# Kernel optimization log

Hardware: AMD Instinct MI355X
Metric: run time of the kernel (lower is better)

The kernel has to match this reference:

```python
import jax, jax.numpy as jnp
import numpy as np

N_Q_HEADS = 16
N_KV_HEADS = 4
HEAD_DIM = 128
SLIDING_WINDOW = 1024
ROPE_BASE = 1024


def _rope_tables(L, dim):
    # half-truncate RoPE: first dim//4 freqs geometric, next dim//4 zero
    freqs = (1.0 / ROPE_BASE) ** jnp.linspace(0.0, 1.0, num=dim // 4)
    freqs = jnp.concatenate([freqs, jnp.zeros(dim // 4, dtype=freqs.dtype)])
    theta = jnp.arange(L, dtype=jnp.float32)[:, None] * freqs[None, :]  # (L, dim/2)
    cos = jnp.cos(theta)[None, :, None, :]  # (1, L, 1, dim/2)
    sin = jnp.sin(theta)[None, :, None, :]
    return cos, sin


def _rotate(x, cos, sin):
    # x: (B, L, H, D)
    x1, x2 = jnp.split(x, 2, axis=-1)
    return jnp.concatenate([x1 * cos + x2 * sin, -x1 * sin + x2 * cos], axis=-1)


def setup_inputs() -> dict:
    key = jax.random.key(0)
    k1, k2, k3, k4 = jax.random.split(key, 4)
    B, L, D = 1, 2048, 2048
    qkv_dim = (N_Q_HEADS + 2 * N_KV_HEADS) * HEAD_DIM  # 3072
    return {
        "x": jax.random.normal(k1, (B, L, D), dtype=jnp.float32),
        "Wqkv": jax.random.normal(k2, (D, qkv_dim), dtype=jnp.float32) * (D ** -0.5),
        "Wo": jax.random.normal(k3, (N_Q_HEADS * HEAD_DIM, D), dtype=jnp.float32) * ((N_Q_HEADS * HEAD_DIM) ** -0.5),
        "s": jax.random.normal(k4, (1, N_Q_HEADS), dtype=jnp.float32) * 0.1,
    }


def reference(x, Wqkv, Wo, s):
    B, L, D = x.shape
    H, QM, hd = N_KV_HEADS, N_Q_HEADS // N_KV_HEADS, HEAD_DIM

    proj = x @ Wqkv  # (B, L, (Hq + 2*Hkv) * hd)
    q, k, v = jnp.split(proj, (N_Q_HEADS * hd, (N_Q_HEADS + N_KV_HEADS) * hd), axis=-1)

    cos, sin = _rope_tables(L, hd)
    q = _rotate(q.reshape(B, L, -1, hd), cos, sin).reshape(B, L, H, QM, hd)
    k = _rotate(k.reshape(B, L, H, hd), cos, sin)
    v = v.reshape(B, L, H, hd)

    sm_scale = 1.0 / jnp.sqrt(jnp.float32(hd))
    q_pos = jnp.arange(L)[None, :, None]
    k_pos = jnp.arange(L)[None, None, :]
    causal = q_pos >= k_pos                       # (1, L, L)
    window = q_pos < k_pos + SLIDING_WINDOW       # index % 2 == 0 -> window active
    mask = causal & window

    # (B, H, M, Lq, Lk) attention logits
    attn = jnp.einsum("bqhmd,bkhd->bhmqk", q, k) * sm_scale
    # NOTE: faithful to source: -inf placed WHERE mask is True
    attn = jnp.where(mask, -jnp.inf, attn)

    sink = jnp.broadcast_to(s.reshape(B, H, QM, 1, 1), (B, H, QM, L, 1))
    w = jax.nn.softmax(jnp.concatenate([attn, sink], axis=-1), axis=-1)[..., :-1]

    out = jnp.einsum("bhmqk,bkhd->bqhmd", w, v).reshape(B, L, -1)
    return out @ Wo
```

## Files before the change

### kernel.cpp

```cpp
#include <hip/hip_runtime.h>
#include <hip/hip_bf16.h>
#include <math.h>

typedef __bf16 bf16;
typedef __bf16 bf16x8 __attribute__((ext_vector_type(8)));
typedef __bf16 bf16x4v __attribute__((ext_vector_type(4)));
typedef short s16x4 __attribute__((ext_vector_type(4)));
typedef float f32x4 __attribute__((ext_vector_type(4)));

#define GLD16(gp, lp) __builtin_amdgcn_global_load_lds( \
    (__attribute__((address_space(1))) void*)(void*)(gp), \
    (__attribute__((address_space(3))) void*)(lp), 16, 0, 0)

#define L_SEQ 2048
#define D_MODEL 2048
#define QKV_N 3072
#define HD 128
#define QSCALE 0.1275310242959836f
#define LOG2E 1.4426950408889634f

__global__ __launch_bounds__(256) void prep(const float* __restrict__ x,
                                            const float* __restrict__ Wqkv,
                                            const float* __restrict__ Wo,
                                            bf16* __restrict__ xb,
                                            bf16* __restrict__ wqkvT,
                                            bf16* __restrict__ woT) {
    __shared__ float tile[32][33];
    int bid = blockIdx.x;
    if (bid < 4096) {
        int idx = (bid * 256 + threadIdx.x) * 4;
        float4 f = *(const float4*)(x + idx);
        bf16x4v o;
        o.x = (bf16)f.x; o.y = (bf16)f.y; o.z = (bf16)f.z; o.w = (bf16)f.w;
        *(bf16x4v*)(xb + idx) = o;
        return;
    }
    bid -= 4096;
    const float* src; bf16* dst; long ld_s, ld_d; int bx, by;
    if (bid < 6144) { bx = bid % 96; by = bid / 96; src = Wqkv; dst = wqkvT; ld_s = QKV_N; ld_d = D_MODEL; }
    else { bid -= 6144; bx = bid & 63; by = bid >> 6; src = Wo; dst = woT; ld_s = D_MODEL; ld_d = D_MODEL; }
    const int tx = threadIdx.x & 31, ty = threadIdx.x >> 5;
    const long c = bx * 32 + tx, r0 = by * 32;
#pragma unroll
    for (int i = 0; i < 4; ++i)
        tile[ty + i * 8][tx] = src[(r0 + ty + i * 8) * ld_s + c];
    __syncthreads();
    const long c0 = bx * 32;
#pragma unroll
    for (int i = 0; i < 4; ++i)
        dst[(c0 + ty + i * 8) * ld_d + r0 + tx] = (bf16)tile[tx][ty + i * 8];
}

__global__ __launch_bounds__(256, 3) void gemm_qkv(const bf16* __restrict__ A,
                                                   const bf16* __restrict__ Bt,
                                                   bf16* __restrict__ Qb,
                                                   bf16* __restrict__ Kb,
                                                   bf16* __restrict__ Vtb) {
    constexpr int KDIM = D_MODEL;
    __shared__ __align__(16) bf16 As[2][64 * 64];
    __shared__ __align__(16) bf16 Bs[2][128 * 64];
    const int tid = threadIdx.x;
    const int wid = tid >> 6, lane = tid & 63;
    const int quad = lane >> 4, l15 = lane & 15;
    const int wm = wid & 1, wn = wid >> 1;
    const int head = blockIdx.x;
    const long m0 = (long)blockIdx.y * 64, n0 = (long)head * 128;

    f32x4 acc[2][4];
#pragma unroll
    for (int i = 0; i < 2; ++i)
#pragma unroll
        for (int j = 0; j < 4; ++j) acc[i][j] = (f32x4){0.f, 0.f, 0.f, 0.f};

    const int srow8 = lane >> 3;
    const int schunk = lane & 7;

    auto stage = [&](int k0, int buf) {
#pragma unroll
        for (int ii = 0; ii < 2; ++ii) {
            const int rowb = wid * 16 + ii * 8;
            const int row = rowb + srow8;
            const int gcol = (schunk ^ (row & 7)) * 8;
            GLD16(A + (m0 + row) * KDIM + k0 + gcol, &As[buf][rowb * 64]);
        }
#pragma unroll
        for (int ii = 0; ii < 4; ++ii) {
            const int rowb = wid * 32 + ii * 8;
            const int row = rowb + srow8;
            const int gcol = (schunk ^ (row & 7)) * 8;
            GLD16(Bt + (n0 + row) * KDIM + k0 + gcol, &Bs[buf][rowb * 64]);
        }
    };
    stage(0, 0);

    for (int k0 = 0; k0 < KDIM; k0 += 64) {
        __syncthreads();
        if (k0 + 64 < KDIM) stage(k0 + 64, ((k0 >> 6) + 1) & 1);
        const int buf = (k0 >> 6) & 1;
#pragma unroll
        for (int ks = 0; ks < 2; ++ks) {
            const int pos = ((ks * 4 + quad) ^ (l15 & 7)) * 8;
            bf16x8 af[2], bfr[4];
#pragma unroll
            for (int i = 0; i < 2; ++i)
                af[i] = *(const bf16x8*)&As[buf][(wm * 32 + i * 16 + l15) * 64 + pos];
#pragma unroll
            for (int j = 0; j < 4; ++j)
                bfr[j] = *(const bf16x8*)&Bs[buf][(j * 32 + wn * 16 + l15) * 64 + pos];
#pragma unroll
            for (int i = 0; i < 2; ++i)
#pragma unroll
                for (int j = 0; j < 4; ++j)
                    acc[i][j] = __builtin_amdgcn_mfma_f32_16x16x32_bf16(af[i], bfr[j], acc[i][j], 0, 0, 0);
        }
    }

    if (head < 20) {
        const float sc = head < 16 ? QSCALE : 1.0f;
        bf16* dst = head < 16 ? Qb + (long)head * L_SEQ * HD
                              : Kb + (long)(head - 16) * L_SEQ * HD;
        const int d0 = wn * 16 + l15;
        const float freq = exp2f((float)d0 * (-10.0f / 31.0f));
        const int d1 = 32 + wn * 16 + l15;
#pragma unroll
        for (int i = 0; i < 2; ++i)
#pragma unroll
            for (int r = 0; r < 4; ++r) {
                const long row = m0 + wm * 32 + i * 16 + quad * 4 + r;
                float sn, cs;
                sincosf((float)row * freq, &sn, &cs);
                const float x1 = acc[i][0][r], x2 = acc[i][2][r];
                bf16* p = dst + row * HD;
                p[d0]      = (bf16)((x1 * cs + x2 * sn) * sc);
                p[d0 + 64] = (bf16)((x2 * cs - x1 * sn) * sc);
                p[d1]      = (bf16)(acc[i][1][r] * sc);
                p[d1 + 64] = (bf16)(acc[i][3][r] * sc);
            }
    } else {
        bf16* dst = Vtb + (long)(head - 20) * HD * L_SEQ;
#pragma unroll
        for (int i = 0; i < 2; ++i) {
            const long m = m0 + wm * 32 + i * 16 + quad * 4;
#pragma unroll
            for (int j = 0; j < 4; ++j) {
                const int d = j * 32 + wn * 16 + l15;
                bf16x4v vv;
#pragma unroll
                for (int r = 0; r < 4; ++r) vv[r] = (bf16)acc[i][j][r];
                *(bf16x4v*)(dst + (long)d * L_SEQ + m) = vv;
            }
        }
    }
}

__global__ __launch_bounds__(256, 3) void gemm_out(const bf16* __restrict__ A,
                                                   const bf16* __restrict__ Bt,
                                                   float* __restrict__ C) {
    constexpr int KDIM = D_MODEL;
    __shared__ __align__(16) bf16 As[2][64 * 64];
    __shared__ __align__(16) bf16 Bs[2][128 * 64];
    const int tid = threadIdx.x;
    const int wid = tid >> 6, lane = tid & 63;
    const int quad = lane >> 4, l15 = lane & 15;
    const int wm = wid & 1, wn = wid >> 1;
    const long m0 = (long)blockIdx.y * 64, n0 = (long)blockIdx.x * 128;

    f32x4 acc[2][4];
#pragma unroll
    for (int i = 0; i < 2; ++i)
#pragma unroll
        for (int j = 0; j < 4; ++j) acc[i][j] = (f32x4){0.f, 0.f, 0.f, 0.f};

    const int srow8 = lane >> 3;
    const int schunk = lane & 7;

    auto stage = [&](int k0, int buf) {
#pragma unroll
        for (int ii = 0; ii < 2; ++ii) {
            const int rowb = wid * 16 + ii * 8;
            const int row = rowb + srow8;
            const int gcol = (schunk ^ (row & 7)) * 8;
            GLD16(A + (m0 + row) * KDIM + k0 + gcol, &As[buf][rowb * 64]);
        }
#pragma unroll
        for (int ii = 0; ii < 4; ++ii) {
            const int rowb = wid * 32 + ii * 8;
            const int row = rowb + srow8;
            const int gcol = (schunk ^ (row & 7)) * 8;
            GLD16(Bt + (n0 + row) * KDIM + k0 + gcol, &Bs[buf][rowb * 64]);
        }
    };
    stage(0, 0);

    for (int k0 = 0; k0 < KDIM; k0 += 64) {
        __syncthreads();
        if (k0 + 64 < KDIM) stage(k0 + 64, ((k0 >> 6) + 1) & 1);
        const int buf = (k0 >> 6) & 1;
#pragma unroll
        for (int ks = 0; ks < 2; ++ks) {
            const int pos = ((ks * 4 + quad) ^ (l15 & 7)) * 8;
            bf16x8 af[2], bfr[4];
#pragma unroll
            for (int i = 0; i < 2; ++i)
                af[i] = *(const bf16x8*)&As[buf][(wm * 32 + i * 16 + l15) * 64 + pos];
#pragma unroll
            for (int j = 0; j < 4; ++j)
                bfr[j] = *(const bf16x8*)&Bs[buf][(j * 32 + wn * 16 + l15) * 64 + pos];
#pragma unroll
            for (int i = 0; i < 2; ++i)
#pragma unroll
                for (int j = 0; j < 4; ++j)
                    acc[i][j] = __builtin_amdgcn_mfma_f32_16x16x32_bf16(af[i], bfr[j], acc[i][j], 0, 0, 0);
        }
    }

#pragma unroll
    for (int i = 0; i < 2; ++i)
#pragma unroll
        for (int j = 0; j < 4; ++j) {
            const long row = m0 + wm * 32 + i * 16 + quad * 4;
            const long col = n0 + j * 32 + wn * 16 + l15;
#pragma unroll
            for (int r = 0; r < 4; ++r)
                C[(row + r) * (long)D_MODEL + col] = acc[i][j][r];
        }
}

__global__ __launch_bounds__(256, 2) void attn_p(const bf16* __restrict__ Qb,
                                                 const bf16* __restrict__ Kb,
                                                 const bf16* __restrict__ Vtb,
                                                 bf16* __restrict__ Opart,
                                                 float* __restrict__ lpart) {
    __shared__ __align__(1024) char smem[65536];

    const int bid = blockIdx.x;
    int t, hq, half;
    if (bid < 256) { t = bid >> 5; hq = (bid & 31) >> 1; half = bid & 1; }
    else { int b2 = bid - 256; t = 8 + (b2 >> 5); hq = (b2 & 31) >> 1; half = b2 & 1; }
    const int h = hq >> 2;
    const int q0 = t * 128;
    const int tid = threadIdx.x;
    const int w = tid >> 6;
    const int lane = tid & 63;
    const int quad = lane >> 4, l15 = lane & 15;

    const bf16* Qg = Qb + (long)hq * L_SEQ * HD;
    const bf16* Kg = Kb + (long)h * L_SEQ * HD;
    const bf16* Vg = Vtb + (long)h * HD * L_SEQ;

    bf16x8 qb[2][4];
#pragma unroll
    for (int rf = 0; rf < 2; ++rf)
#pragma unroll
        for (int kkd = 0; kkd < 4; ++kkd)
            qb[rf][kkd] = *(const bf16x8*)(Qg + (long)(q0 + w * 32 + rf * 16 + l15) * HD
                                              + kkd * 32 + quad * 8);

    f32x4 oaccT[2][8];
#pragma unroll
    for (int rf = 0; rf < 2; ++rf)
#pragma unroll
        for (int j = 0; j < 8; ++j) oaccT[rf][j] = (f32x4){0.f, 0.f, 0.f, 0.f};
    float lacc[2] = {0.f, 0.f};

    const int locnt = (2 * t - 14 > 0) ? (2 * t - 14) : 0;
    const int n = locnt + 32 - 2 * t;
    const int cnt = n >> 1;

    auto ktile = [&](int idx) {
        const int i = 2 * idx + half;
        return (i < locnt) ? i : (2 * t + (i - locnt));
    };

    auto stage = [&](int idx, int buf) {
        const int k0 = ktile(idx) * 64;
        bf16* Ksb  = (bf16*)(smem + buf * 32768);
        bf16* Vtsb = (bf16*)(smem + buf * 32768 + 16384);
#pragma unroll
        for (int ii = 0; ii < 4; ++ii) {
            int rowb = w * 16 + ii * 4;
            int row = rowb + quad;
            GLD16(Kg + (long)(k0 + row) * HD + ((l15 ^ (row & 7)) * 8), &Ksb[rowb * 128]);
        }
#pragma unroll
        for (int ii = 0; ii < 4; ++ii) {
            int rowb = w * 32 + ii * 8;
            int row = rowb + (lane >> 3);
            GLD16(Vg + (long)row * L_SEQ + k0 + (((lane & 7) ^ (row & 7)) * 8), &Vtsb[rowb * 64]);
        }
    };

    stage(0, 0);

    for (int it = 0; it < cnt; ++it) {
        __syncthreads();
        if (it + 1 < cnt) stage(it + 1, (it + 1) & 1);

        const int kt = ktile(it);
        const int k0 = kt * 64;
        const bf16* Ks  = (const bf16*)(smem + (it & 1) * 32768);
        const bf16* Vts = (const bf16*)(smem + (it & 1) * 32768 + 16384);

        f32x4 sacc[2][4];
#pragma unroll
        for (int kb = 0; kb < 4; ++kb) {
            bf16x8 ka[4];
#pragma unroll
            for (int kkd = 0; kkd < 4; ++kkd)
                ka[kkd] = *(const bf16x8*)&Ks[(kb * 16 + l15) * 128 +
                                              (((kkd * 4 + quad) ^ (l15 & 7)) * 8)];
#pragma unroll
            for (int rf = 0; rf < 2; ++rf) {
                f32x4 acc = (f32x4){0.f, 0.f, 0.f, 0.f};
#pragma unroll
                for (int kkd = 0; kkd < 4; ++kkd)
                    acc = __builtin_amdgcn_mfma_f32_16x16x32_bf16(ka[kkd], qb[rf][kkd], acc, 0, 0, 0);
                sacc[rf][kb] = acc;
            }
        }

        const bool bnd = (kt == 2 * t) || (kt == 2 * t + 1) ||
                         (kt == 2 * t - 15) || (kt == 2 * t - 16);
        s16x4 pb[2][4];
#pragma unroll
        for (int rf = 0; rf < 2; ++rf) {
            const int qq = q0 + w * 32 + rf * 16 + l15;
#pragma unroll
            for (int kb = 0; kb < 4; ++kb) {
#pragma unroll
                for (int r = 0; r < 4; ++r) {
                    float v = sacc[rf][kb][r];
                    if (bnd) {
                        const int kk = k0 + kb * 16 + quad * 4 + r;
                        if (!((kk > qq) || (kk <= qq - 1024))) v = -1e30f;
                    }
                    const float p = exp2f(v);
                    lacc[rf] += p;
                    bf16 hp = (bf16)p;
                    pb[rf][kb][r] = __builtin_bit_cast(short, hp);
                }
            }
        }

#pragma unroll
        for (int j = 0; j < 8; ++j) {
            const int drow = j * 16 + l15;
#pragma unroll
            for (int kq = 0; kq < 4; ++kq) {
                const int pc = ((kq * 2 + (quad >> 1)) ^ (l15 & 7));
                s16x4 va = *(const s16x4*)((const char*)&Vts[drow * 64] + pc * 16 + (quad & 1) * 8);
#pragma unroll
                for (int rf = 0; rf < 2; ++rf)
                    oaccT[rf][j] = __builtin_amdgcn_mfma_f32_16x16x16bf16_1k(
                        va, pb[rf][kq], oaccT[rf][j], 0, 0, 0);
            }
        }
    }

#pragma unroll
    for (int rf = 0; rf < 2; ++rf) {
        lacc[rf] += __shfl_xor(lacc[rf], 16, 64);
        lacc[rf] += __shfl_xor(lacc[rf], 32, 64);
    }

    bf16* Od = Opart + (long)bid * 16384;
#pragma unroll
    for (int rf = 0; rf < 2; ++rf) {
        const int ql = w * 32 + rf * 16 + l15;
#pragma unroll
        for (int j = 0; j < 8; ++j) {
            bf16x4v ov;
#pragma unroll
            for (int r = 0; r < 4; ++r) ov[r] = (bf16)oaccT[rf][j][r];
            *(bf16x4v*)(Od + ql * 128 + j * 16 + quad * 4) = ov;
        }
        if (quad == 0) lpart[bid * 128 + ql] = lacc[rf];
    }
}

__global__ __launch_bounds__(256) void attn_combine(const bf16* __restrict__ Opart,
                                                    const float* __restrict__ lpart,
                                                    const float* __restrict__ sink,
                                                    bf16* __restrict__ attnb) {
    const int job = blockIdx.x >> 3, sub = blockIdx.x & 7;
    const int t = job >> 4, hq = job & 15;
    const int bid0 = (t < 8) ? (t * 32 + hq * 2) : (256 + (t - 8) * 32 + hq * 2);
    const int bid1 = bid0 + 1;
    const int e = sub * 2048 + threadIdx.x * 8;
    const int q = e >> 7, d0 = e & 127;
    bf16x8 o0 = *(const bf16x8*)(Opart + (long)bid0 * 16384 + q * 128 + d0);
    bf16x8 o1 = *(const bf16x8*)(Opart + (long)bid1 * 16384 + q * 128 + d0);
    const float l = lpart[bid0 * 128 + q] + lpart[bid1 * 128 + q] +
                    exp2f(sink[hq] * LOG2E);
    const float inv = 1.0f / l;
    bf16x8 ov;
#pragma unroll
    for (int r = 0; r < 8; ++r)
        ov[r] = (bf16)(((float)o0[r] + (float)o1[r]) * inv);
    *(bf16x8*)(attnb + (long)(t * 128 + q) * D_MODEL + hq * 128 + d0) = ov;
}

extern "C" void kernel_launch(void* const* d_in, const int* in_sizes, int n_in,
                              void* d_out, int out_size, void* d_ws, size_t ws_size,
                              hipStream_t stream) {
    (void)in_sizes; (void)n_in; (void)out_size; (void)ws_size;
    const float* x    = (const float*)d_in[0];
    const float* Wqkv = (const float*)d_in[1];
    const float* Wo   = (const float*)d_in[2];
    const float* s    = (const float*)d_in[3];
    float* out = (float*)d_out;

    char* ws = (char*)d_ws;
    bf16* xb    = (bf16*)ws;
    bf16* wqkvT = (bf16*)(ws + 8388608);
    bf16* Qb    = (bf16*)(ws + 20971520);
    bf16* Kb    = (bf16*)(ws + 29360128);
    bf16* Vtb   = (bf16*)(ws + 31457280);
    bf16* woT   = (bf16*)(ws + 33554432);
    bf16* attnb = (bf16*)(ws + 41943040);
    bf16* Opart = (bf16*)ws;
    float* lpart = (float*)(ws + 16777216);

    prep<<<14336, 256, 0, stream>>>(x, Wqkv, Wo, xb, wqkvT, woT);

    gemm_qkv<<<dim3(QKV_N / 128, L_SEQ / 64), 256, 0, stream>>>(
        xb, wqkvT, Qb, Kb, Vtb);

    attn_p<<<512, 256, 0, stream>>>(Qb, Kb, Vtb, Opart, lpart);

    attn_combine<<<2048, 256, 0, stream>>>(Opart, lpart, s, attnb);

    gemm_out<<<dim3(D_MODEL / 128, L_SEQ / 64), 256, 0, stream>>>(
        attnb, woT, out);
}
```

Before: 218.4 us.

## Split attention KV range four ways with 32-key tiles and higher occupancy

Each attention job is now split across four blocks instead of two, using 32-key tiles and half the shared memory so that four blocks can be resident per CU. The partial outputs are spread over the output buffer and the workspace, and the combine kernel sums four partials. s_setprio is raised around the MFMA sections so waves in the matrix phase get issue priority. The aim is more parallelism and better latency hiding, paid for with more partial-output traffic and a larger per-tile overhead share.

```diff
diff --git a/kernel.cpp b/kernel.cpp
--- a/kernel.cpp
+++ b/kernel.cpp
@@ -226,17 +226,17 @@
         }
 }
 
-__global__ __launch_bounds__(256, 2) void attn_p(const bf16* __restrict__ Qb,
+__global__ __launch_bounds__(256, 4) void attn_p(const bf16* __restrict__ Qb,
                                                  const bf16* __restrict__ Kb,
                                                  const bf16* __restrict__ Vtb,
-                                                 bf16* __restrict__ Opart,
+                                                 bf16* __restrict__ O0,
+                                                 bf16* __restrict__ O1,
                                                  float* __restrict__ lpart) {
-    __shared__ __align__(1024) char smem[65536];
-
-    const int bid = blockIdx.x;
-    int t, hq, half;
-    if (bid < 256) { t = bid >> 5; hq = (bid & 31) >> 1; half = bid & 1; }
-    else { int b2 = bid - 256; t = 8 + (b2 >> 5); hq = (b2 & 31) >> 1; half = b2 & 1; }
+    __shared__ __align__(1024) char smem[32768];
+
+    const int pbid = blockIdx.x;
+    const int job = pbid >> 2, qtr = pbid & 3;
+    const int t = job >> 4, hq = job & 15;
     const int h = hq >> 2;
     const int q0 = t * 128;
     const int tid = threadIdx.x;
@@ -263,30 +263,31 @@
         for (int j = 0; j < 8; ++j) oaccT[rf][j] = (f32x4){0.f, 0.f, 0.f, 0.f};
     float lacc[2] = {0.f, 0.f};
 
-    const int locnt = (2 * t - 14 > 0) ? (2 * t - 14) : 0;
-    const int n = locnt + 32 - 2 * t;
-    const int cnt = n >> 1;
+    const int locnt = (4 * t - 28 > 0) ? (4 * t - 28) : 0;
+    const int n32 = locnt + 64 - 4 * t;
+    const int cnt = (n32 - qtr + 3) >> 2;
 
     auto ktile = [&](int idx) {
-        const int i = 2 * idx + half;
-        return (i < locnt) ? i : (2 * t + (i - locnt));
+        const int i = 4 * idx + qtr;
+        return (i < locnt) ? i : (4 * t + (i - locnt));
     };
 
     auto stage = [&](int idx, int buf) {
-        const int k0 = ktile(idx) * 64;
-        bf16* Ksb  = (bf16*)(smem + buf * 32768);
-        bf16* Vtsb = (bf16*)(smem + buf * 32768 + 16384);
-#pragma unroll
-        for (int ii = 0; ii < 4; ++ii) {
-            int rowb = w * 16 + ii * 4;
-            int row = rowb + quad;
+        const int k0 = ktile(idx) * 32;
+        bf16* Ksb  = (bf16*)(smem + buf * 16384);
+        bf16* Vtsb = (bf16*)(smem + buf * 16384 + 8192);
+#pragma unroll
+        for (int ii = 0; ii < 2; ++ii) {
+            const int rowb = w * 8 + ii * 4;
+            const int row = rowb + quad;
             GLD16(Kg + (long)(k0 + row) * HD + ((l15 ^ (row & 7)) * 8), &Ksb[rowb * 128]);
         }
 #pragma unroll
-        for (int ii = 0; ii < 4; ++ii) {
-            int rowb = w * 32 + ii * 8;
-            int row = rowb + (lane >> 3);
-            GLD16(Vg + (long)row * L_SEQ + k0 + (((lane & 7) ^ (row & 7)) * 8), &Vtsb[rowb * 64]);
+        for (int ii = 0; ii < 2; ++ii) {
+            const int rowb = w * 32 + ii * 16;
+            const int row = rowb + (lane >> 2);
+            GLD16(Vg + (long)row * L_SEQ + k0 + (((lane & 3) ^ ((row >> 1) & 3)) * 8),
+                  &Vtsb[rowb * 32]);
         }
     };
 
@@ -297,13 +298,14 @@
         if (it + 1 < cnt) stage(it + 1, (it + 1) & 1);
 
         const int kt = ktile(it);
-        const int k0 = kt * 64;
-        const bf16* Ks  = (const bf16*)(smem + (it & 1) * 32768);
-        const bf16* Vts = (const bf16*)(smem + (it & 1) * 32768 + 16384);
-
-        f32x4 sacc[2][4];
-#pragma unroll
-        for (int kb = 0; kb < 4; ++kb) {
+        const int k0 = kt * 32;
+        const bf16* Ks  = (const bf16*)(smem + (it & 1) * 16384);
+        const bf16* Vts = (const bf16*)(smem + (it & 1) * 16384 + 8192);
+
+        f32x4 sacc[2][2];
+        __builtin_amdgcn_s_setprio(1);
+#pragma unroll
+        for (int kb = 0; kb < 2; ++kb) {
             bf16x8 ka[4];
 #pragma unroll
             for (int kkd = 0; kkd < 4; ++kkd)
@@ -318,15 +320,16 @@
                 sacc[rf][kb] = acc;
             }
         }
-
-        const bool bnd = (kt == 2 * t) || (kt == 2 * t + 1) ||
-                         (kt == 2 * t - 15) || (kt == 2 * t - 16);
-        s16x4 pb[2][4];
+        __builtin_amdgcn_s_setprio(0);
+
+        const bool bnd = (kt >= 4 * t && kt < 4 * t + 4) ||
+                         (kt >= 4 * t - 32 && kt <= 4 * t - 29);
+        s16x4 pb[2][2];
 #pragma unroll
         for (int rf = 0; rf < 2; ++rf) {
             const int qq = q0 + w * 32 + rf * 16 + l15;
 #pragma unroll
-            for (int kb = 0; kb < 4; ++kb) {
+            for (int kb = 0; kb < 2; ++kb) {
 #pragma unroll
                 for (int r = 0; r < 4; ++r) {
                     float v = sacc[rf][kb][r];
@@ -342,19 +345,21 @@
             }
         }
 
+        __builtin_amdgcn_s_setprio(1);
 #pragma unroll
         for (int j = 0; j < 8; ++j) {
             const int drow = j * 16 + l15;
 #pragma unroll
-            for (int kq = 0; kq < 4; ++kq) {
-                const int pc = ((kq * 2 + (quad >> 1)) ^ (l15 & 7));
-                s16x4 va = *(const s16x4*)((const char*)&Vts[drow * 64] + pc * 16 + (quad & 1) * 8);
+            for (int kq = 0; kq < 2; ++kq) {
+                const int pc = (kq * 2 + (quad >> 1)) ^ ((drow >> 1) & 3);
+                s16x4 va = *(const s16x4*)((const char*)&Vts[drow * 32] + pc * 16 + (quad & 1) * 8);
 #pragma unroll
                 for (int rf = 0; rf < 2; ++rf)
                     oaccT[rf][j] = __builtin_amdgcn_mfma_f32_16x16x16bf16_1k(
                         va, pb[rf][kq], oaccT[rf][j], 0, 0, 0);
             }
         }
+        __builtin_amdgcn_s_setprio(0);
     }
 
 #pragma unroll
@@ -363,7 +368,8 @@
         lacc[rf] += __shfl_xor(lacc[rf], 32, 64);
     }
 
-    bf16* Od = Opart + (long)bid * 16384;
+    bf16* Od = (pbid < 512) ? O0 + (long)pbid * 16384
+                            : O1 + (long)(pbid - 512) * 16384;
 #pragma unroll
     for (int rf = 0; rf < 2; ++rf) {
         const int ql = w * 32 + rf * 16 + l15;
@@ -374,29 +380,37 @@
             for (int r = 0; r < 4; ++r) ov[r] = (bf16)oaccT[rf][j][r];
             *(bf16x4v*)(Od + ql * 128 + j * 16 + quad * 4) = ov;
         }
-        if (quad == 0) lpart[bid * 128 + ql] = lacc[rf];
-    }
-}
-
-__global__ __launch_bounds__(256) void attn_combine(const bf16* __restrict__ Opart,
+        if (quad == 0) lpart[pbid * 128 + ql] = lacc[rf];
+    }
+}
+
+__global__ __launch_bounds__(256) void attn_combine(const bf16* __restrict__ O0,
+                                                    const bf16* __restrict__ O1,
                                                     const float* __restrict__ lpart,
                                                     const float* __restrict__ sink,
                                                     bf16* __restrict__ attnb) {
     const int job = blockIdx.x >> 3, sub = blockIdx.x & 7;
     const int t = job >> 4, hq = job & 15;
-    const int bid0 = (t < 8) ? (t * 32 + hq * 2) : (256 + (t - 8) * 32 + hq * 2);
-    const int bid1 = bid0 + 1;
+    const bf16* Ob = (job < 128) ? O0 + (long)job * 65536
+                                 : O1 + (long)(job - 128) * 65536;
     const int e = sub * 2048 + threadIdx.x * 8;
     const int q = e >> 7, d0 = e & 127;
-    bf16x8 o0 = *(const bf16x8*)(Opart + (long)bid0 * 16384 + q * 128 + d0);
-    bf16x8 o1 = *(const bf16x8*)(Opart + (long)bid1 * 16384 + q * 128 + d0);
-    const float l = lpart[bid0 * 128 + q] + lpart[bid1 * 128 + q] +
-                    exp2f(sink[hq] * LOG2E);
+    float acc[8];
+#pragma unroll
+    for (int r = 0; r < 8; ++r) acc[r] = 0.f;
+    float l = exp2f(sink[hq] * LOG2E);
+#pragma unroll
+    for (int s = 0; s < 4; ++s) {
+        bf16x8 o = *(const bf16x8*)(Ob + (long)s * 16384 + q * 128 + d0);
+#pragma unroll
+        for (int r = 0; r < 8; ++r) acc[r] += (float)o[r];
+        l += lpart[(job * 4 + s) * 128 + q];
+    }
     const float inv = 1.0f / l;
     bf16x8 ov;
 #pragma unroll
     for (int r = 0; r < 8; ++r)
-        ov[r] = (bf16)(((float)o0[r] + (float)o1[r]) * inv);
+        ov[r] = (bf16)(acc[r] * inv);
     *(bf16x8*)(attnb + (long)(t * 128 + q) * D_MODEL + hq * 128 + d0) = ov;
 }
 
@@ -418,7 +432,8 @@
     bf16* Vtb   = (bf16*)(ws + 31457280);
     bf16* woT   = (bf16*)(ws + 33554432);
     bf16* attnb = (bf16*)(ws + 41943040);
-    bf16* Opart = (bf16*)ws;
+    bf16* Opart0 = (bf16*)out;
+    bf16* Opart1 = (bf16*)ws;
     float* lpart = (float*)(ws + 16777216);
 
     prep<<<14336, 256, 0, stream>>>(x, Wqkv, Wo, xb, wqkvT, woT);
@@ -426,9 +441,9 @@
     gemm_qkv<<<dim3(QKV_N / 128, L_SEQ / 64), 256, 0, stream>>>(
         xb, wqkvT, Qb, Kb, Vtb);
 
-    attn_p<<<512, 256, 0, stream>>>(Qb, Kb, Vtb, Opart, lpart);
-
-    attn_combine<<<2048, 256, 0, stream>>>(Opart, lpart, s, attnb);
+    attn_p<<<1024, 256, 0, stream>>>(Qb, Kb, Vtb, Opart0, Opart1, lpart);
+
+    attn_combine<<<2048, 256, 0, stream>>>(Opart0, Opart1, lpart, s, attnb);
 
     gemm_out<<<dim3(D_MODEL / 128, L_SEQ / 64), 256, 0, stream>>>(
         attnb, woT, out);
```

Result: slower. 309.2 us (+41.6%).

## Use 8 waves per attention block with 16 query rows each and MFMA priority

Applied to the files above, without the earlier changes.

The attention kernel now runs 512 threads per block. Each of its 8 waves handles 16 query rows instead of 32, which halves the per-thread register arrays for Q fragments, accumulators and probabilities and lets more waves be resident. K/V staging is split across the larger thread count. s_setprio is raised around the MFMA phases so waves doing matrix work get scheduler priority over the softmax phase. The trade-off is that each K fragment read from LDS is now reused for one query fragment instead of two, so LDS traffic per FLOP doubles.

```diff
diff --git a/kernel.cpp b/kernel.cpp
--- a/kernel.cpp
+++ b/kernel.cpp
@@ -226,7 +226,7 @@
         }
 }
 
-__global__ __launch_bounds__(256, 2) void attn_p(const bf16* __restrict__ Qb,
+__global__ __launch_bounds__(512, 4) void attn_p(const bf16* __restrict__ Qb,
                                                  const bf16* __restrict__ Kb,
                                                  const bf16* __restrict__ Vtb,
                                                  bf16* __restrict__ Opart,
@@ -248,20 +248,16 @@
     const bf16* Kg = Kb + (long)h * L_SEQ * HD;
     const bf16* Vg = Vtb + (long)h * HD * L_SEQ;
 
-    bf16x8 qb[2][4];
-#pragma unroll
-    for (int rf = 0; rf < 2; ++rf)
-#pragma unroll
-        for (int kkd = 0; kkd < 4; ++kkd)
-            qb[rf][kkd] = *(const bf16x8*)(Qg + (long)(q0 + w * 32 + rf * 16 + l15) * HD
-                                              + kkd * 32 + quad * 8);
-
-    f32x4 oaccT[2][8];
-#pragma unroll
-    for (int rf = 0; rf < 2; ++rf)
-#pragma unroll
-        for (int j = 0; j < 8; ++j) oaccT[rf][j] = (f32x4){0.f, 0.f, 0.f, 0.f};
-    float lacc[2] = {0.f, 0.f};
+    bf16x8 qb[4];
+#pragma unroll
+    for (int kkd = 0; kkd < 4; ++kkd)
+        qb[kkd] = *(const bf16x8*)(Qg + (long)(q0 + w * 16 + l15) * HD
+                                      + kkd * 32 + quad * 8);
+
+    f32x4 oaccT[8];
+#pragma unroll
+    for (int j = 0; j < 8; ++j) oaccT[j] = (f32x4){0.f, 0.f, 0.f, 0.f};
+    float lacc = 0.f;
 
     const int locnt = (2 * t - 14 > 0) ? (2 * t - 14) : 0;
     const int n = locnt + 32 - 2 * t;
@@ -277,14 +273,14 @@
         bf16* Ksb  = (bf16*)(smem + buf * 32768);
         bf16* Vtsb = (bf16*)(smem + buf * 32768 + 16384);
 #pragma unroll
-        for (int ii = 0; ii < 4; ++ii) {
-            int rowb = w * 16 + ii * 4;
+        for (int ii = 0; ii < 2; ++ii) {
+            int rowb = w * 8 + ii * 4;
             int row = rowb + quad;
             GLD16(Kg + (long)(k0 + row) * HD + ((l15 ^ (row & 7)) * 8), &Ksb[rowb * 128]);
         }
 #pragma unroll
-        for (int ii = 0; ii < 4; ++ii) {
-            int rowb = w * 32 + ii * 8;
+        for (int ii = 0; ii < 2; ++ii) {
+            int rowb = w * 16 + ii * 8;
             int row = rowb + (lane >> 3);
             GLD16(Vg + (long)row * L_SEQ + k0 + (((lane & 7) ^ (row & 7)) * 8), &Vtsb[rowb * 64]);
         }
@@ -301,7 +297,8 @@
         const bf16* Ks  = (const bf16*)(smem + (it & 1) * 32768);
         const bf16* Vts = (const bf16*)(smem + (it & 1) * 32768 + 16384);
 
-        f32x4 sacc[2][4];
+        f32x4 sacc[4];
+        __builtin_amdgcn_s_setprio(1);
 #pragma unroll
         for (int kb = 0; kb < 4; ++kb) {
             bf16x8 ka[4];
@@ -309,39 +306,37 @@
             for (int kkd = 0; kkd < 4; ++kkd)
                 ka[kkd] = *(const bf16x8*)&Ks[(kb * 16 + l15) * 128 +
                                               (((kkd * 4 + quad) ^ (l15 & 7)) * 8)];
-#pragma unroll
-            for (int rf = 0; rf < 2; ++rf) {
-                f32x4 acc = (f32x4){0.f, 0.f, 0.f, 0.f};
-#pragma unroll
-                for (int kkd = 0; kkd < 4; ++kkd)
-                    acc = __builtin_amdgcn_mfma_f32_16x16x32_bf16(ka[kkd], qb[rf][kkd], acc, 0, 0, 0);
-                sacc[rf][kb] = acc;
-            }
-        }
+            f32x4 acc = (f32x4){0.f, 0.f, 0.f, 0.f};
+#pragma unroll
+            for (int kkd = 0; kkd < 4; ++kkd)
+                acc = __builtin_amdgcn_mfma_f32_16x16x32_bf16(ka[kkd], qb[kkd], acc, 0, 0, 0);
+            sacc[kb] = acc;
+        }
+        __builtin_amdgcn_s_setprio(0);
 
         const bool bnd = (kt == 2 * t) || (kt == 2 * t + 1) ||
                          (kt == 2 * t - 15) || (kt == 2 * t - 16);
-        s16x4 pb[2][4];
-#pragma unroll
-        for (int rf = 0; rf < 2; ++rf) {
-            const int qq = q0 + w * 32 + rf * 16 + l15;
+        s16x4 pb[4];
+        {
+            const int qq = q0 + w * 16 + l15;
 #pragma unroll
             for (int kb = 0; kb < 4; ++kb) {
 #pragma unroll
                 for (int r = 0; r < 4; ++r) {
-                    float v = sacc[rf][kb][r];
+                    float v = sacc[kb][r];
                     if (bnd) {
                         const int kk = k0 + kb * 16 + quad * 4 + r;
                         if (!((kk > qq) || (kk <= qq - 1024))) v = -1e30f;
                     }
                     const float p = exp2f(v);
-                    lacc[rf] += p;
+                    lacc += p;
                     bf16 hp = (bf16)p;
-                    pb[rf][kb][r] = __builtin_bit_cast(short, hp);
+                    pb[kb][r] = __builtin_bit_cast(short, hp);
                 }
             }
         }
 
+        __builtin_amdgcn_s_setprio(1);
 #pragma unroll
         for (int j = 0; j < 8; ++j) {
             const int drow = j * 16 + l15;
@@ -349,32 +344,27 @@
             for (int kq = 0; kq < 4; ++kq) {
                 const int pc = ((kq * 2 + (quad >> 1)) ^ (l15 & 7));
                 s16x4 va = *(const s16x4*)((const char*)&Vts[drow * 64] + pc * 16 + (quad & 1) * 8);
-#pragma unroll
-                for (int rf = 0; rf < 2; ++rf)
-                    oaccT[rf][j] = __builtin_amdgcn_mfma_f32_16x16x16bf16_1k(
-                        va, pb[rf][kq], oaccT[rf][j], 0, 0, 0);
+                oaccT[j] = __builtin_amdgcn_mfma_f32_16x16x16bf16_1k(
+                    va, pb[kq], oaccT[j], 0, 0, 0);
             }
         }
-    }
-
-#pragma unroll
-    for (int rf = 0; rf < 2; ++rf) {
-        lacc[rf] += __shfl_xor(lacc[rf], 16, 64);
-        lacc[rf] += __shfl_xor(lacc[rf], 32, 64);
-    }
+        __builtin_amdgcn_s_setprio(0);
+    }
+
+    lacc += __shfl_xor(lacc, 16, 64);
+    lacc += __shfl_xor(lacc, 32, 64);
 
     bf16* Od = Opart + (long)bid * 16384;
-#pragma unroll
-    for (int rf = 0; rf < 2; ++rf) {
-        const int ql = w * 32 + rf * 16 + l15;
+    {
+        const int ql = w * 16 + l15;
 #pragma unroll
         for (int j = 0; j < 8; ++j) {
             bf16x4v ov;
 #pragma unroll
-            for (int r = 0; r < 4; ++r) ov[r] = (bf16)oaccT[rf][j][r];
+            for (int r = 0; r < 4; ++r) ov[r] = (bf16)oaccT[j][r];
             *(bf16x4v*)(Od + ql * 128 + j * 16 + quad * 4) = ov;
         }
-        if (quad == 0) lpart[bid * 128 + ql] = lacc[rf];
+        if (quad == 0) lpart[bid * 128 + ql] = lacc;
     }
 }
 
@@ -426,7 +416,7 @@
     gemm_qkv<<<dim3(QKV_N / 128, L_SEQ / 64), 256, 0, stream>>>(
         xb, wqkvT, Qb, Kb, Vtb);
 
-    attn_p<<<512, 256, 0, stream>>>(Qb, Kb, Vtb, Opart, lpart);
+    attn_p<<<512, 512, 0, stream>>>(Qb, Kb, Vtb, Opart, lpart);
 
     attn_combine<<<2048, 256, 0, stream>>>(Opart, lpart, s, attnb);
 
```

Result: slower. 222.9 us (+2.1%).

## Split attention waves across query and key halves to halve LDS operand reads

Applied to the files above, without the earlier changes.

The four waves of the sliding-window attention kernel are re-partitioned into 2 query groups × 2 key groups. Each wave now handles 64 query rows against 32 keys per tile, instead of 32 rows against all 64 keys. Each wave therefore reads half as much K and V from LDS per tile while reusing its Q fragments and P values across more MFMAs. The two key-half partial outputs are summed through shared memory at the end, and both partial row sums are written to a doubled lpart layout that the combine kernel now reads. The change also raises MFMA wave priority around the matrix loops, at the cost of doubling the accumulator registers (128 floats per lane), which risks spills or reduced occupancy under the 2-blocks launch bound.

```diff
diff --git a/kernel.cpp b/kernel.cpp
--- a/kernel.cpp
+++ b/kernel.cpp
@@ -241,6 +241,7 @@
     const int q0 = t * 128;
     const int tid = threadIdx.x;
     const int w = tid >> 6;
+    const int wk = w & 1, wq = w >> 1;
     const int lane = tid & 63;
     const int quad = lane >> 4, l15 = lane & 15;
 
@@ -248,20 +249,20 @@
     const bf16* Kg = Kb + (long)h * L_SEQ * HD;
     const bf16* Vg = Vtb + (long)h * HD * L_SEQ;
 
-    bf16x8 qb[2][4];
-#pragma unroll
-    for (int rf = 0; rf < 2; ++rf)
+    bf16x8 qb[4][4];
+#pragma unroll
+    for (int rf = 0; rf < 4; ++rf)
 #pragma unroll
         for (int kkd = 0; kkd < 4; ++kkd)
-            qb[rf][kkd] = *(const bf16x8*)(Qg + (long)(q0 + w * 32 + rf * 16 + l15) * HD
+            qb[rf][kkd] = *(const bf16x8*)(Qg + (long)(q0 + wq * 64 + rf * 16 + l15) * HD
                                               + kkd * 32 + quad * 8);
 
-    f32x4 oaccT[2][8];
-#pragma unroll
-    for (int rf = 0; rf < 2; ++rf)
+    f32x4 oaccT[4][8];
+#pragma unroll
+    for (int rf = 0; rf < 4; ++rf)
 #pragma unroll
         for (int j = 0; j < 8; ++j) oaccT[rf][j] = (f32x4){0.f, 0.f, 0.f, 0.f};
-    float lacc[2] = {0.f, 0.f};
+    float lacc[4] = {0.f, 0.f, 0.f, 0.f};
 
     const int locnt = (2 * t - 14 > 0) ? (2 * t - 14) : 0;
     const int n = locnt + 32 - 2 * t;
@@ -301,37 +302,41 @@
         const bf16* Ks  = (const bf16*)(smem + (it & 1) * 32768);
         const bf16* Vts = (const bf16*)(smem + (it & 1) * 32768 + 16384);
 
-        f32x4 sacc[2][4];
-#pragma unroll
-        for (int kb = 0; kb < 4; ++kb) {
-            bf16x8 ka[4];
+        bf16x8 ka[2][4];
+#pragma unroll
+        for (int kb = 0; kb < 2; ++kb)
 #pragma unroll
             for (int kkd = 0; kkd < 4; ++kkd)
-                ka[kkd] = *(const bf16x8*)&Ks[(kb * 16 + l15) * 128 +
-                                              (((kkd * 4 + quad) ^ (l15 & 7)) * 8)];
-#pragma unroll
-            for (int rf = 0; rf < 2; ++rf) {
+                ka[kb][kkd] = *(const bf16x8*)&Ks[(wk * 32 + kb * 16 + l15) * 128 +
+                                                  (((kkd * 4 + quad) ^ (l15 & 7)) * 8)];
+
+        f32x4 sacc[4][2];
+        __builtin_amdgcn_s_setprio(1);
+#pragma unroll
+        for (int rf = 0; rf < 4; ++rf)
+#pragma unroll
+            for (int kb = 0; kb < 2; ++kb) {
                 f32x4 acc = (f32x4){0.f, 0.f, 0.f, 0.f};
 #pragma unroll
                 for (int kkd = 0; kkd < 4; ++kkd)
-                    acc = __builtin_amdgcn_mfma_f32_16x16x32_bf16(ka[kkd], qb[rf][kkd], acc, 0, 0, 0);
+                    acc = __builtin_amdgcn_mfma_f32_16x16x32_bf16(ka[kb][kkd], qb[rf][kkd], acc, 0, 0, 0);
                 sacc[rf][kb] = acc;
             }
-        }
+        __builtin_amdgcn_s_setprio(0);
 
         const bool bnd = (kt == 2 * t) || (kt == 2 * t + 1) ||
                          (kt == 2 * t - 15) || (kt == 2 * t - 16);
-        s16x4 pb[2][4];
-#pragma unroll
-        for (int rf = 0; rf < 2; ++rf) {
-            const int qq = q0 + w * 32 + rf * 16 + l15;
-#pragma unroll
-            for (int kb = 0; kb < 4; ++kb) {
+        s16x4 pb[4][2];
+#pragma unroll
+        for (int rf = 0; rf < 4; ++rf) {
+            const int qq = q0 + wq * 64 + rf * 16 + l15;
+#pragma unroll
+            for (int kb = 0; kb < 2; ++kb) {
 #pragma unroll
                 for (int r = 0; r < 4; ++r) {
                     float v = sacc[rf][kb][r];
                     if (bnd) {
-                        const int kk = k0 + kb * 16 + quad * 4 + r;
+                        const int kk = k0 + wk * 32 + kb * 16 + quad * 4 + r;
                         if (!((kk > qq) || (kk <= qq - 1024))) v = -1e30f;
                     }
                     const float p = exp2f(v);
@@ -342,39 +347,61 @@
             }
         }
 
+        __builtin_amdgcn_s_setprio(1);
 #pragma unroll
         for (int j = 0; j < 8; ++j) {
             const int drow = j * 16 + l15;
 #pragma unroll
-            for (int kq = 0; kq < 4; ++kq) {
-                const int pc = ((kq * 2 + (quad >> 1)) ^ (l15 & 7));
+            for (int kq = 0; kq < 2; ++kq) {
+                const int pc = (wk * 4 + kq * 2 + (quad >> 1)) ^ (l15 & 7);
                 s16x4 va = *(const s16x4*)((const char*)&Vts[drow * 64] + pc * 16 + (quad & 1) * 8);
 #pragma unroll
-                for (int rf = 0; rf < 2; ++rf)
+                for (int rf = 0; rf < 4; ++rf)
                     oaccT[rf][j] = __builtin_amdgcn_mfma_f32_16x16x16bf16_1k(
                         va, pb[rf][kq], oaccT[rf][j], 0, 0, 0);
             }
         }
-    }
-
-#pragma unroll
-    for (int rf = 0; rf < 2; ++rf) {
+        __builtin_amdgcn_s_setprio(0);
+    }
+
+#pragma unroll
+    for (int rf = 0; rf < 4; ++rf) {
         lacc[rf] += __shfl_xor(lacc[rf], 16, 64);
         lacc[rf] += __shfl_xor(lacc[rf], 32, 64);
     }
 
+    __syncthreads();
+    if (wk) {
+        float* xch = (float*)smem;
+#pragma unroll
+        for (int rf = 0; rf < 4; ++rf)
+#pragma unroll
+            for (int j = 0; j < 8; ++j)
+                *(f32x4*)(xch + ((wq * 32 + rf * 8 + j) * 64 + lane) * 4) = oaccT[rf][j];
+    }
+    __syncthreads();
+
     bf16* Od = Opart + (long)bid * 16384;
-#pragma unroll
-    for (int rf = 0; rf < 2; ++rf) {
-        const int ql = w * 32 + rf * 16 + l15;
-#pragma unroll
-        for (int j = 0; j < 8; ++j) {
-            bf16x4v ov;
-#pragma unroll
-            for (int r = 0; r < 4; ++r) ov[r] = (bf16)oaccT[rf][j][r];
-            *(bf16x4v*)(Od + ql * 128 + j * 16 + quad * 4) = ov;
-        }
-        if (quad == 0) lpart[bid * 128 + ql] = lacc[rf];
+    if (!wk) {
+        const float* xch = (const float*)smem;
+#pragma unroll
+        for (int rf = 0; rf < 4; ++rf) {
+            const int ql = wq * 64 + rf * 16 + l15;
+#pragma unroll
+            for (int j = 0; j < 8; ++j) {
+                f32x4 o = *(const f32x4*)(xch + ((wq * 32 + rf * 8 + j) * 64 + lane) * 4);
+                o += oaccT[rf][j];
+                bf16x4v ov;
+#pragma unroll
+                for (int r = 0; r < 4; ++r) ov[r] = (bf16)o[r];
+                *(bf16x4v*)(Od + ql * 128 + j * 16 + quad * 4) = ov;
+            }
+        }
+    }
+    if (quad == 0) {
+#pragma unroll
+        for (int rf = 0; rf < 4; ++rf)
+            lpart[bid * 256 + wk * 128 + wq * 64 + rf * 16 + l15] = lacc[rf];
     }
 }
 
@@ -390,7 +417,8 @@
     const int q = e >> 7, d0 = e & 127;
     bf16x8 o0 = *(const bf16x8*)(Opart + (long)bid0 * 16384 + q * 128 + d0);
     bf16x8 o1 = *(const bf16x8*)(Opart + (long)bid1 * 16384 + q * 128 + d0);
-    const float l = lpart[bid0 * 128 + q] + lpart[bid1 * 128 + q] +
+    const float l = lpart[bid0 * 256 + q] + lpart[bid0 * 256 + 128 + q] +
+                    lpart[bid1 * 256 + q] + lpart[bid1 * 256 + 128 + q] +
                     exp2f(sink[hq] * LOG2E);
     const float inv = 1.0f / l;
     bf16x8 ov;
```

New measurement: 269.2 us. +23.3%, slower.
